# Optimization experiments

Hardware: AMD Instinct MI355X
Metric: run time of the kernel (lower is better)

## Reference

```python
import jax, jax.numpy as jnp
import numpy as np
from jax import lax

V, EMB, ENH, DNH, ZD, K = 51, 64, 256, 256, 32, 512
B, T = 1024, 128


def gru_scan(xs, h0, Wih, Whh, bih, bhh, collect):
    """PyTorch-convention GRU. xs: [T,B,D], h0: [B,H]. Returns (ys or None, hT)."""
    def step(h, x):
        gi = x @ Wih.T + bih          # [B, 3H]
        gh = h @ Whh.T + bhh          # [B, 3H]
        ir, iz, inn = jnp.split(gi, 3, axis=-1)
        hr, hz, hn = jnp.split(gh, 3, axis=-1)
        r = jax.nn.sigmoid(ir + hr)
        zg = jax.nn.sigmoid(iz + hz)
        n = jnp.tanh(inn + r * hn)
        hnew = (1.0 - zg) * n + zg * h
        return hnew, (hnew if collect else None)
    hT, ys = lax.scan(step, h0, xs)
    return ys, hT


def setup_inputs() -> dict:
    key = jax.random.key(0)
    ks = jax.random.split(key, 24)
    w = lambda k, shape, s=0.1: (jax.random.normal(k, shape, jnp.float32) * s)
    inp = {
        "x": jax.random.randint(ks[0], (B, T), 0, V),
        "emb_enc": w(ks[1], (V, EMB)),
        "emb_dec": w(ks[2], (V, EMB)),
        # encoder bidirectional GRU (fwd + bwd directions)
        "Wih_f": w(ks[3], (3 * ENH, EMB)), "Whh_f": w(ks[4], (3 * ENH, ENH)),
        "bih_f": w(ks[5], (3 * ENH,)), "bhh_f": w(ks[6], (3 * ENH,)),
        "Wih_b": w(ks[7], (3 * ENH, EMB)), "Whh_b": w(ks[8], (3 * ENH, ENH)),
        "bih_b": w(ks[9], (3 * ENH,)), "bhh_b": w(ks[10], (3 * ENH,)),
        # down_to_z: Linear(2*ENC_NH -> Z_NH)
        "Wdown": w(ks[11], (ZD, 2 * ENH)), "bdown": w(ks[12], (ZD,)),
        # VQ codebook, uniform(-1/K, 1/K) as in source
        "codebook": jax.random.uniform(ks[13], (K, ZD), jnp.float32, -1.0 / K, 1.0 / K),
        # up_from_z: Linear(Z_NH -> DEC_NH)
        "Wup": w(ks[14], (DNH, ZD)), "bup": w(ks[15], (DNH,)),
        # decoder GRU: input = INPUT_EMB_DIM + Z_NH
        "Wih_d": w(ks[16], (3 * DNH, EMB + ZD)), "Whh_d": w(ks[17], (3 * DNH, DNH)),
        "bih_d": w(ks[18], (3 * DNH,)), "bhh_d": w(ks[19], (3 * DNH,)),
        # output projection Linear(DEC_NH -> VOCABSIZE)
        "Wout": w(ks[20], (V, DNH)), "bout": w(ks[21], (V,)),
    }
    return inp


def reference(x, emb_enc, emb_dec, Wih_f, Whh_f, bih_f, bhh_f,
              Wih_b, Whh_b, bih_b, bhh_b, Wdown, bdown, codebook,
              Wup, bup, Wih_d, Whh_d, bih_d, bhh_d, Wout, bout):
    sg = lax.stop_gradient
    Bsz, Tlen = x.shape

    # ---- Encoder: bidirectional GRU, keep final hidden of each direction ----
    e = emb_enc[x]                              # [B,T,EMB]
    xs = jnp.transpose(e, (1, 0, 2))            # [T,B,EMB]
    h0 = jnp.zeros((Bsz, ENH), e.dtype)
    _, hf = gru_scan(xs, h0, Wih_f, Whh_f, bih_f, bhh_f, collect=False)
    _, hb = gru_scan(xs[::-1], h0, Wih_b, Whh_b, bih_b, bhh_b, collect=False)
    out_h = jnp.concatenate([hf, hb], axis=-1)  # [B, 2*ENH]

    # ---- down to z ----
    z = out_h @ Wdown.T + bdown                 # [B, ZD]

    # ---- VQ quantizer ----
    d2 = (z ** 2).sum(-1, keepdims=True) + (codebook ** 2).sum(-1) - 2.0 * (z @ codebook.T)  # [B,K]
    idx = jnp.argmin(d2, axis=-1)               # [B]
    quantized = codebook[idx]                   # [B, ZD]
    commit = ((sg(quantized) - z) ** 2).mean(-1)
    embed_l = ((quantized - sg(z)) ** 2).mean(-1)
    qloss = 0.1 * commit + 0.1 * embed_l
    Q = jnp.sum(qloss)
    qz = z + sg(quantized - z)                  # straight-through [B, ZD]

    # ---- up to decoder hidden ----
    hidden = qz @ Wup.T + bup                   # [B, DNH]

    # ---- Decoder GRU over src, z concatenated at every step ----
    src, tgt = x[:, :-1], x[:, 1:]
    d = emb_dec[src]                            # [B,T-1,EMB]
    zrep = jnp.broadcast_to(qz[:, None, :], (Bsz, Tlen - 1, ZD))
    dec_in = jnp.concatenate([zrep, d], axis=-1)            # [B,T-1,EMB+ZD]
    ys, _ = gru_scan(jnp.transpose(dec_in, (1, 0, 2)), hidden,
                     Wih_d, Whh_d, bih_d, bhh_d, collect=True)  # [T-1,B,DNH]
    logits = jnp.transpose(ys, (1, 0, 2)) @ Wout.T + bout   # [B,T-1,V]

    # cross entropy, reduction='sum', ignore_index=0
    logp = jax.nn.log_softmax(logits, axis=-1)
    nll = -jnp.take_along_axis(logp, tgt[..., None], axis=-1).squeeze(-1)  # [B,T-1]
    mask = (tgt != 0)
    xloss = jnp.sum(nll * mask)
    nonpadded_tokens = jnp.sum(mask)
    pred_tokens = jnp.argmax(logits, axis=-1)

    return (xloss, nonpadded_tokens, pred_tokens, Q, idx[:, None])
```

## Files before the change

### kernel.cpp

```cpp
#include <hip/hip_runtime.h>
#include <cstdint>

typedef unsigned short u16;
typedef unsigned int u32;
typedef __attribute__((ext_vector_type(4))) int int4v;
typedef __attribute__((ext_vector_type(8))) short short8;
typedef __attribute__((ext_vector_type(4))) float f32x4;

#define XLOSS_OFF 0
#define NPAD_OFF  1
#define PRED_OFF  2
#define Q_OFF     130050
#define IDX_OFF   130051

__device__ __forceinline__ u16 f2b(float f){
  union { float f; unsigned int i; } c; c.f = f;
  unsigned int i = c.i;
  unsigned int r = (i + 0x7FFFu + ((i >> 16) & 1u)) >> 16;
  return (u16)r;
}

#define LOG2E 1.442695040889634f
__device__ __forceinline__ float fast_sigmoid(float x){
  return __builtin_amdgcn_rcpf(1.f + __builtin_amdgcn_exp2f(-LOG2E*x));
}
__device__ __forceinline__ float fast_tanh(float x){
  return 1.f - 2.f*__builtin_amdgcn_rcpf(1.f + __builtin_amdgcn_exp2f((2.f*LOG2E)*x));
}

__global__ __launch_bounds__(256) void k_prep_wo(
    const float* __restrict__ Wo, u16* __restrict__ oWo, float* __restrict__ dout){
  int idx = blockIdx.x*256 + threadIdx.x;
  if (idx == 0){ dout[XLOSS_OFF]=0.f; dout[NPAD_OFF]=0.f; dout[Q_OFF]=0.f; }
  int row = idx >> 8, k = idx & 255;
  oWo[idx] = (row < 51) ? f2b(Wo[row*256 + k]) : (u16)0;
}

__global__ __launch_bounds__(64) void k_prep_q(
    const float* __restrict__ Wf, const float* __restrict__ Wb, const float* __restrict__ Wd,
    signed char* __restrict__ qf, signed char* __restrict__ qb, signed char* __restrict__ qd,
    float* __restrict__ invf, float* __restrict__ invb, float* __restrict__ invd){
  const int row = blockIdx.x;
  const int mat = row / 768, r = row - mat*768;
  const float* W = (mat==0 ? Wf : (mat==1 ? Wb : Wd)) + (size_t)r*256;
  signed char* q = (mat==0 ? qf : (mat==1 ? qb : qd)) + (size_t)r*256;
  float* inv     = (mat==0 ? invf : (mat==1 ? invb : invd));
  const int lane = threadIdx.x;
  float4 v = *(const float4*)(W + lane*4);
  float m = fmaxf(fmaxf(fabsf(v.x),fabsf(v.y)), fmaxf(fabsf(v.z),fabsf(v.w)));
  #pragma unroll
  for (int off=32; off>0; off>>=1) m = fmaxf(m, __shfl_xor(m, off));
  m = fmaxf(m, 1e-20f);
  const float s = 127.f / m;
  int a0 = __float2int_rn(v.x*s), a1 = __float2int_rn(v.y*s);
  int a2 = __float2int_rn(v.z*s), a3 = __float2int_rn(v.w*s);
  u32 packed = (a0&255) | ((a1&255)<<8) | ((a2&255)<<16) | ((a3&255)<<24);
  *(u32*)(q + lane*4) = packed;
  if (lane == 0) inv[r] = m * (1.f/127.f);
}

__global__ __launch_bounds__(256) void k_prep_g(
    const float* __restrict__ emb_e, const float* __restrict__ emb_d,
    const float* __restrict__ Wih_f, const float* __restrict__ bih_f, const float* __restrict__ bhh_f,
    const float* __restrict__ Wih_b, const float* __restrict__ bih_b, const float* __restrict__ bhh_b,
    const float* __restrict__ Wih_d,
    float* __restrict__ Gf, float* __restrict__ Gb, float* __restrict__ Gd){
  int idx = blockIdx.x*256 + threadIdx.x;
  int tab = idx / 39168;
  int rem = idx - tab*39168;
  int v = rem / 768;
  int n = rem - v*768;
  float acc = 0.f;
  if (tab == 0){
    const float* e = emb_e + v*64; const float* w = Wih_f + n*64;
    for (int k=0;k<64;k++) acc += e[k]*w[k];
    acc += bih_f[n] + (n < 512 ? bhh_f[n] : 0.f);
    Gf[rem] = acc;
  } else if (tab == 1){
    const float* e = emb_e + v*64; const float* w = Wih_b + n*64;
    for (int k=0;k<64;k++) acc += e[k]*w[k];
    acc += bih_b[n] + (n < 512 ? bhh_b[n] : 0.f);
    Gb[rem] = acc;
  } else {
    const float* e = emb_d + v*64; const float* w = Wih_d + n*96 + 32;
    for (int k=0;k<64;k++) acc += e[k]*w[k];
    Gd[rem] = acc;
  }
}

template<int MODE>
__global__ __launch_bounds__(512)
__attribute__((amdgpu_waves_per_eu(2, 2)))
void k_gru(
    const signed char* __restrict__ W0, const signed char* __restrict__ W1,
    const float* __restrict__ I0, const float* __restrict__ I1,
    const float* __restrict__ G0, const float* __restrict__ G1,
    const float* __restrict__ bhh0, const float* __restrict__ bhh1,
    const int* __restrict__ x,
    const float* __restrict__ zc, const float* __restrict__ h0g,
    float* __restrict__ out_h, u16* __restrict__ ys){
  __shared__ signed char hbf[2*4096];
  __shared__ int xsh[1024];
  __shared__ int gh[8*772];
  __shared__ float zcs[(MODE==1) ? 8*768 : 4];

  const int tid = threadIdx.x;
  const int lane = tid & 63;
  const int wave = tid >> 6;
  const int l15 = lane & 15, lhi = lane >> 4;

  bool fwd = true; int gb;
  const signed char* W; const float* G; const float* bhh; const float* invS;
  if (MODE == 0){
    int bi = blockIdx.x;
    fwd = bi < 128; gb = fwd ? bi : bi - 128;
    W = fwd ? W0 : W1; G = fwd ? G0 : G1; bhh = fwd ? bhh0 : bhh1;
    invS = fwd ? I0 : I1;
  } else {
    gb = blockIdx.x; W = W0; G = G0; bhh = bhh0; invS = I0;
  }
  const int b0 = gb * 8;
  const int nT = (MODE == 0) ? 128 : 127;
  const float HS    = (MODE == 0) ? 127.f : 63.f;
  const float invHS = (MODE == 0) ? (1.f/127.f) : (1.f/63.f);

  int4v wq[6][4];
  #pragma unroll
  for (int g=0; g<3; g++){
    #pragma unroll
    for (int hh=0; hh<2; hh++){
      const signed char* p = W + (size_t)(g*256 + wave*32 + hh*16 + l15)*256 + lhi*16;
      #pragma unroll
      for (int kt=0; kt<4; kt++)
        wq[g*2+hh][kt] = *(const int4v*)(p + kt*64);
    }
  }
  #pragma unroll
  for (int kt=0; kt<4; kt++){
    asm volatile("" : "+v"(wq[0][kt]));
    asm volatile("" : "+v"(wq[1][kt]));
    asm volatile("" : "+v"(wq[2][kt]));
    asm volatile("" : "+v"(wq[3][kt]));
    asm volatile("" : "+v"(wq[4][kt]));
    asm volatile("" : "+v"(wq[5][kt]));
  }

  const int gm = wave;
  const int c4 = lane * 4;
  f32x4 isr4 = *(const f32x4*)(invS + c4);
  f32x4 isz4 = *(const f32x4*)(invS + 256 + c4);
  f32x4 isn4 = *(const f32x4*)(invS + 512 + c4);
  #pragma unroll
  for (int i=0;i<4;i++){ isr4[i] *= invHS; isz4[i] *= invHS; isn4[i] *= invHS; }
  const f32x4 bn4 = *(const f32x4*)(bhh + 512 + c4);

  for (int i = tid; i < 1024; i += 512) xsh[i] = x[b0*128 + i];
  for (int i = tid*4; i < 8192; i += 2048) *(int*)&hbf[i] = 0;
  if (MODE == 1){
    const f32x4* src = (const f32x4*)(zc + (size_t)b0*768);
    f32x4* dst = (f32x4*)zcs;
    for (int i = tid; i < 1536; i += 512) dst[i] = src[i];
  }
  __syncthreads();

  float hreg[4];
  #pragma unroll
  for (int i=0;i<4;i++) hreg[i] = 0.f;
  if (MODE == 1){
    f32x4 h0v = *(const f32x4*)(h0g + (size_t)(b0+gm)*256 + c4);
    u32 pk = 0;
    #pragma unroll
    for (int i=0;i<4;i++){
      hreg[i] = h0v[i];
      int q = __float2int_rn(fminf(fmaxf(h0v[i]*HS, -127.f), 127.f));
      pk |= (u32)(q & 255) << (8*i);
    }
    *(u32*)&hbf[gm*256 + (c4 ^ (gm<<4))] = pk;
  }
  __syncthreads();

  int aoff[4];
  #pragma unroll
  for (int kt=0; kt<4; kt++)
    aoff[kt] = l15*256 + ((kt*64 + lhi*16) ^ (l15<<4));

  int cur = 0;
  for (int t=0; t<nT; ++t){
    const int te = (MODE==0 && !fwd) ? (127 - t) : t;
    const int tok = xsh[(gm<<7) + te];
    const float* Gp = G + (size_t)tok*768 + c4;
    f32x4 gr4 = *(const f32x4*)(Gp);
    f32x4 gz4 = *(const f32x4*)(Gp + 256);
    f32x4 gn4 = *(const f32x4*)(Gp + 512);

    const signed char* hb = hbf + (cur<<12);
    int4v af[4];
    #pragma unroll
    for (int kt=0; kt<4; kt++) af[kt] = *(const int4v*)(hb + aoff[kt]);

    int4v acc[6];
    #pragma unroll
    for (int j=0;j<6;j++) acc[j] = (int4v){0,0,0,0};
    #pragma unroll
    for (int kt=0; kt<4; kt++)
      #pragma unroll
      for (int j=0;j<6;j++)
        acc[j] = __builtin_amdgcn_mfma_i32_16x16x64_i8(af[kt], wq[j][kt], acc[j], 0,0,0);

    if (lhi < 2){
      #pragma unroll
      for (int j=0;j<6;j++){
        const int g = j >> 1;
        const int col = wave*32 + (j&1)*16 + l15;
        #pragma unroll
        for (int r=0;r<4;r++)
          gh[(4*lhi+r)*772 + g*256 + col] = acc[j][r];
      }
    }
    __syncthreads();

    int4v hiR = *(const int4v*)&gh[gm*772 + c4];
    int4v hiZ = *(const int4v*)&gh[gm*772 + 256 + c4];
    int4v hiN = *(const int4v*)&gh[gm*772 + 512 + c4];
    f32x4 zr4 = {0.f,0.f,0.f,0.f}, zz4 = zr4, zn4 = zr4;
    if (MODE == 1){
      zr4 = *(const f32x4*)&zcs[gm*768 + c4];
      zz4 = *(const f32x4*)&zcs[gm*768 + 256 + c4];
      zn4 = *(const f32x4*)&zcs[gm*768 + 512 + c4];
    }
    u32 pk = 0;
    #pragma unroll
    for (int i=0;i<4;i++){
      float gr = gr4[i] + zr4[i];
      float gz = gz4[i] + zz4[i];
      float gn = gn4[i] + zn4[i];
      float rg = fast_sigmoid((float)hiR[i]*isr4[i] + gr);
      float zg = fast_sigmoid((float)hiZ[i]*isz4[i] + gz);
      float nn = fast_tanh(gn + rg*((float)hiN[i]*isn4[i] + bn4[i]));
      float hv = nn + zg*(hreg[i] - nn);
      hreg[i] = hv;
      int q = __float2int_rn(fminf(fmaxf(hv*HS, -127.f), 127.f));
      pk |= (u32)(q & 255) << (8*i);
    }
    *(u32*)&hbf[((cur^1)<<12) + gm*256 + (c4 ^ (gm<<4))] = pk;
    if (MODE == 1){
      u32 lo = (u32)f2b(hreg[0]) | ((u32)f2b(hreg[1]) << 16);
      u32 hi = (u32)f2b(hreg[2]) | ((u32)f2b(hreg[3]) << 16);
      uint2 v; v.x = lo; v.y = hi;
      *(uint2*)&ys[((size_t)(b0+gm)*127 + t)*256 + c4] = v;
    }
    __syncthreads();
    cur ^= 1;
  }

  if (MODE == 0){
    f32x4 o = {hreg[0], hreg[1], hreg[2], hreg[3]};
    *(f32x4*)(out_h + (size_t)(b0+gm)*512 + (fwd ? 0 : 256) + c4) = o;
  }
}

__global__ __launch_bounds__(64) void k_vq(
    const float* __restrict__ outH, const float* __restrict__ Wdown, const float* __restrict__ bdown,
    const float* __restrict__ cb, const float* __restrict__ Wup, const float* __restrict__ bup,
    const float* __restrict__ Wihd, const float* __restrict__ bihd, const float* __restrict__ bhhd,
    float* __restrict__ hidden, float* __restrict__ zc, float* __restrict__ dout){
  const int b = blockIdx.x;
  const int lane = threadIdx.x;
  __shared__ float oh[512];
  __shared__ float zsh[32];
  __shared__ float qsh[32];
  {
    const float* src = outH + (size_t)b*512 + lane*8;
    *(float4*)&oh[lane*8]   = *(const float4*)src;
    *(float4*)&oh[lane*8+4] = *(const float4*)(src+4);
  }
  __syncthreads();
  if (lane < 32){
    float acc = bdown[lane];
    const float* wr = Wdown + lane*512;
    for (int k=0;k<512;k++) acc += wr[k]*oh[k];
    zsh[lane] = acc;
  }
  __syncthreads();
  float bd = 3.4e38f; int bi = 0;
  for (int c8=0;c8<8;c8++){
    const int c = lane*8 + c8;
    const float* cr = cb + c*32;
    float d = 0.f;
    #pragma unroll
    for (int k=0;k<32;k++){ float df = zsh[k]-cr[k]; d += df*df; }
    if (d < bd){ bd = d; bi = c; }
  }
  #pragma unroll
  for (int offm=32; offm>0; offm>>=1){
    float od = __shfl_xor(bd, offm);
    int   oi = __shfl_xor(bi, offm);
    if (od < bd || (od == bd && oi < bi)){ bd = od; bi = oi; }
  }
  if (lane == 0){
    atomicAdd(&dout[Q_OFF], bd * (0.2f/32.f));
    dout[IDX_OFF + b] = (float)bi;
  }
  if (lane < 32) qsh[lane] = cb[(size_t)bi*32 + lane];
  __syncthreads();
  #pragma unroll
  for (int i=0;i<4;i++){
    const int o = lane*4 + i;
    float acc = bup[o];
    const float* wr = Wup + o*32;
    #pragma unroll
    for (int k=0;k<32;k++) acc += wr[k]*qsh[k];
    hidden[(size_t)b*256 + o] = acc;
  }
  #pragma unroll
  for (int i=0;i<12;i++){
    const int o = lane*12 + i;
    float acc = bihd[o] + (o < 512 ? bhhd[o] : 0.f);
    const float* wr = Wihd + (size_t)o*96;
    #pragma unroll
    for (int k=0;k<32;k++) acc += wr[k]*qsh[k];
    zc[(size_t)b*768 + o] = acc;
  }
}

__global__ __launch_bounds__(256) void k_out(
    const u16* __restrict__ ys, const u16* __restrict__ Wo,
    const float* __restrict__ bout, const int* __restrict__ x,
    float* __restrict__ dout){
  const int tid = threadIdx.x;
  const int w = tid >> 6, lane = tid & 63;
  const int l15 = lane & 15, lhi = lane >> 4;
  __shared__ float lg[4][32][66];
  const int rows0 = blockIdx.x*128 + w*32;
  const f32x4 fz = {0.f,0.f,0.f,0.f};
  #pragma unroll
  for (int mt=0; mt<2; mt++){
    const int rb = rows0 + mt*16;
    f32x4 acc[4];
    #pragma unroll
    for (int nt=0;nt<4;nt++) acc[nt] = fz;
    #pragma unroll
    for (int kt=0; kt<8; kt++){
      short8 a = *(const short8*)&ys[(size_t)(rb + l15)*256 + kt*32 + lhi*8];
      #pragma unroll
      for (int nt=0; nt<4; nt++){
        short8 bb = *(const short8*)&Wo[(size_t)(nt*16 + l15)*256 + kt*32 + lhi*8];
        acc[nt] = __builtin_amdgcn_mfma_f32_16x16x32_bf16(a, bb, acc[nt], 0, 0, 0);
      }
    }
    #pragma unroll
    for (int nt=0;nt<4;nt++){
      const int col = nt*16 + l15;
      const float bo = (col < 51) ? bout[col] : 0.f;
      #pragma unroll
      for (int r=0;r<4;r++){
        float v = (col < 51) ? (acc[nt][r] + bo) : -1e30f;
        lg[w][mt*16 + lhi*4 + r][col] = v;
      }
    }
  }
  __syncthreads();
  float xl = 0.f, ct = 0.f;
  if (lane < 32){
    const int grow = rows0 + lane;
    const float* Lr = &lg[w][lane][0];
    float m = Lr[0]; int am = 0;
    for (int i=1;i<51;i++){ float v = Lr[i]; if (v > m){ m = v; am = i; } }
    float s = 0.f;
    for (int i=0;i<51;i++) s += __expf(Lr[i] - m);
    const int bb = grow / 127;
    const int tt = grow - bb*127;
    const int tgt = x[bb*128 + tt + 1];
    const float nll = (m + __logf(s)) - Lr[tgt];
    const float mk = (tgt != 0) ? 1.f : 0.f;
    dout[PRED_OFF + grow] = (float)am;
    xl = nll * mk; ct = mk;
  }
  #pragma unroll
  for (int off=32; off>0; off>>=1){
    xl += __shfl_xor(xl, off);
    ct += __shfl_xor(ct, off);
  }
  if (lane == 0){
    atomicAdd(&dout[XLOSS_OFF], xl);
    atomicAdd(&dout[NPAD_OFF], ct);
  }
}

extern "C" void kernel_launch(void* const* d_in, const int* in_sizes, int n_in,
                              void* d_out, int out_size, void* d_ws, size_t ws_size,
                              hipStream_t stream){
  (void)in_sizes; (void)n_in; (void)out_size; (void)ws_size;
  const int*   x      = (const int*)  d_in[0];
  const float* emb_e  = (const float*)d_in[1];
  const float* emb_d  = (const float*)d_in[2];
  const float* Wih_f  = (const float*)d_in[3];
  const float* Whh_f  = (const float*)d_in[4];
  const float* bih_f  = (const float*)d_in[5];
  const float* bhh_f  = (const float*)d_in[6];
  const float* Wih_b  = (const float*)d_in[7];
  const float* Whh_b  = (const float*)d_in[8];
  const float* bih_b  = (const float*)d_in[9];
  const float* bhh_b  = (const float*)d_in[10];
  const float* Wdown  = (const float*)d_in[11];
  const float* bdown  = (const float*)d_in[12];
  const float* cbook  = (const float*)d_in[13];
  const float* Wup    = (const float*)d_in[14];
  const float* bup    = (const float*)d_in[15];
  const float* Wih_d  = (const float*)d_in[16];
  const float* Whh_d  = (const float*)d_in[17];
  const float* bih_d  = (const float*)d_in[18];
  const float* bhh_d  = (const float*)d_in[19];
  const float* Wout   = (const float*)d_in[20];
  const float* bout   = (const float*)d_in[21];
  float* dout = (float*)d_out;

  char* ws = (char*)d_ws;
  size_t off = 0;
  auto nxt = [&](size_t bytes)->char*{
    char* r = ws + off;
    off += (bytes + 255) & ~(size_t)255;
    return r;
  };
  signed char* Wq_f = (signed char*)nxt((size_t)196608);
  signed char* Wq_b = (signed char*)nxt((size_t)196608);
  signed char* Wq_d = (signed char*)nxt((size_t)196608);
  float* invF = (float*)nxt((size_t)768*4);
  float* invB = (float*)nxt((size_t)768*4);
  float* invD = (float*)nxt((size_t)768*4);
  float* Gf    = (float*)nxt((size_t)39168*4);
  float* Gb    = (float*)nxt((size_t)39168*4);
  float* Gd    = (float*)nxt((size_t)39168*4);
  u16*   Wo_bf = (u16*) nxt((size_t)16384*2);
  float* outH  = (float*)nxt((size_t)524288*4);
  float* hid   = (float*)nxt((size_t)262144*4);
  float* zcw   = (float*)nxt((size_t)786432*4);
  u16*   ysb   = (u16*)  nxt((size_t)33292288*2);

  hipLaunchKernelGGL(k_prep_wo, dim3(64), dim3(256), 0, stream, Wout, Wo_bf, dout);
  hipLaunchKernelGGL(k_prep_q, dim3(2304), dim3(64), 0, stream,
                     Whh_f, Whh_b, Whh_d, Wq_f, Wq_b, Wq_d, invF, invB, invD);
  hipLaunchKernelGGL(k_prep_g, dim3(459), dim3(256), 0, stream,
                     emb_e, emb_d, Wih_f, bih_f, bhh_f, Wih_b, bih_b, bhh_b, Wih_d,
                     Gf, Gb, Gd);
  hipLaunchKernelGGL((k_gru<0>), dim3(256), dim3(512), 0, stream,
                     Wq_f, Wq_b, invF, invB, Gf, Gb, bhh_f, bhh_b, x,
                     (const float*)nullptr, (const float*)nullptr, outH, (u16*)nullptr);
  hipLaunchKernelGGL(k_vq, dim3(1024), dim3(64), 0, stream,
                     outH, Wdown, bdown, cbook, Wup, bup, Wih_d, bih_d, bhh_d,
                     hid, zcw, dout);
  hipLaunchKernelGGL((k_gru<1>), dim3(128), dim3(512), 0, stream,
                     Wq_d, (const signed char*)nullptr, invD, (const float*)nullptr,
                     Gd, (const float*)nullptr, bhh_d, (const float*)nullptr, x,
                     zcw, hid, (float*)nullptr, ysb);
  hipLaunchKernelGGL(k_out, dim3(1016), dim3(256), 0, stream,
                     ysb, Wo_bf, bout, x, dout);
}
```

Baseline: 531.6 us.

## Ping-pong two batch groups per GRU block to overlap MFMA with gate math

The GRU kernel now splits each block's batch rows into two groups, A and B, each with its own hidden-state and gate buffers in shared memory. The recurrent MFMA for one group is issued while the other group runs its sigmoid/tanh gate update, so matrix and vector work can overlap across the per-step barrier. The decoder now uses 2 rows per group and twice as many blocks, to spread its work over more CUs. The cost is that each MFMA tile only fills 2–4 of its 16 rows, and gate outputs and bf16 ys are written per element instead of as packed vector stores.

```diff
diff --git a/kernel.cpp b/kernel.cpp
--- a/kernel.cpp
+++ b/kernel.cpp
@@ -88,7 +88,7 @@
   }
 }
 
-template<int MODE>
+template<int MODE, int GR>
 __global__ __launch_bounds__(512)
 __attribute__((amdgpu_waves_per_eu(2, 2)))
 void k_gru(
@@ -99,10 +99,14 @@
     const int* __restrict__ x,
     const float* __restrict__ zc, const float* __restrict__ h0g,
     float* __restrict__ out_h, u16* __restrict__ ys){
-  __shared__ signed char hbf[2*4096];
-  __shared__ int xsh[1024];
-  __shared__ int gh[8*772];
-  __shared__ float zcs[(MODE==1) ? 8*768 : 4];
+  constexpr int TPR = 512 / GR;
+  constexpr int CPL = 256 / TPR;
+
+  __shared__ signed char hbfA[2*4096];
+  __shared__ signed char hbfB[2*4096];
+  __shared__ int xsh[2*GR*128];
+  __shared__ int ghA[GR*772], ghB[GR*772];
+  __shared__ float zcs[(MODE==1) ? 2*GR*768 : 4];
 
   const int tid = threadIdx.x;
   const int lane = tid & 63;
@@ -112,14 +116,15 @@
   bool fwd = true; int gb;
   const signed char* W; const float* G; const float* bhh; const float* invS;
   if (MODE == 0){
+    const int nblk = 1024 / (2*GR);
     int bi = blockIdx.x;
-    fwd = bi < 128; gb = fwd ? bi : bi - 128;
+    fwd = bi < nblk; gb = fwd ? bi : bi - nblk;
     W = fwd ? W0 : W1; G = fwd ? G0 : G1; bhh = fwd ? bhh0 : bhh1;
     invS = fwd ? I0 : I1;
   } else {
     gb = blockIdx.x; W = W0; G = G0; bhh = bhh0; invS = I0;
   }
-  const int b0 = gb * 8;
+  const int b0 = gb * (2*GR);
   const int nT = (MODE == 0) ? 128 : 127;
   const float HS    = (MODE == 0) ? 127.f : 63.f;
   const float invHS = (MODE == 0) ? (1.f/127.f) : (1.f/63.f);
@@ -145,37 +150,41 @@
     asm volatile("" : "+v"(wq[5][kt]));
   }
 
-  const int gm = wave;
-  const int c4 = lane * 4;
-  f32x4 isr4 = *(const f32x4*)(invS + c4);
-  f32x4 isz4 = *(const f32x4*)(invS + 256 + c4);
-  f32x4 isn4 = *(const f32x4*)(invS + 512 + c4);
-  #pragma unroll
-  for (int i=0;i<4;i++){ isr4[i] *= invHS; isz4[i] *= invHS; isn4[i] *= invHS; }
-  const f32x4 bn4 = *(const f32x4*)(bhh + 512 + c4);
-
-  for (int i = tid; i < 1024; i += 512) xsh[i] = x[b0*128 + i];
-  for (int i = tid*4; i < 8192; i += 2048) *(int*)&hbf[i] = 0;
+  const int gm = tid / TPR;
+  const int ci = (tid % TPR) * CPL;
+  float isr[CPL], isz[CPL], isn[CPL], bnv[CPL];
+  #pragma unroll
+  for (int i=0;i<CPL;i++){
+    isr[i] = invS[ci+i]       * invHS;
+    isz[i] = invS[256 + ci+i] * invHS;
+    isn[i] = invS[512 + ci+i] * invHS;
+    bnv[i] = bhh[512 + ci+i];
+  }
+
+  for (int i = tid; i < 2*GR*128; i += 512) xsh[i] = x[b0*128 + i];
+  for (int i = tid*4; i < 8192; i += 2048){
+    *(int*)&hbfA[i] = 0; *(int*)&hbfB[i] = 0;
+  }
   if (MODE == 1){
     const f32x4* src = (const f32x4*)(zc + (size_t)b0*768);
     f32x4* dst = (f32x4*)zcs;
-    for (int i = tid; i < 1536; i += 512) dst[i] = src[i];
-  }
-  __syncthreads();
-
-  float hreg[4];
-  #pragma unroll
-  for (int i=0;i<4;i++) hreg[i] = 0.f;
+    for (int i = tid; i < 2*GR*192; i += 512) dst[i] = src[i];
+  }
+  __syncthreads();
+
+  float hA[CPL], hB[CPL];
+  #pragma unroll
+  for (int i=0;i<CPL;i++){ hA[i]=0.f; hB[i]=0.f; }
   if (MODE == 1){
-    f32x4 h0v = *(const f32x4*)(h0g + (size_t)(b0+gm)*256 + c4);
-    u32 pk = 0;
-    #pragma unroll
-    for (int i=0;i<4;i++){
-      hreg[i] = h0v[i];
-      int q = __float2int_rn(fminf(fmaxf(h0v[i]*HS, -127.f), 127.f));
-      pk |= (u32)(q & 255) << (8*i);
-    }
-    *(u32*)&hbf[gm*256 + (c4 ^ (gm<<4))] = pk;
+    #pragma unroll
+    for (int i=0;i<CPL;i++){
+      hA[i] = h0g[(size_t)(b0+gm)*256 + ci+i];
+      hB[i] = h0g[(size_t)(b0+GR+gm)*256 + ci+i];
+      int qa = __float2int_rn(fminf(fmaxf(hA[i]*HS, -127.f), 127.f));
+      int qb = __float2int_rn(fminf(fmaxf(hB[i]*HS, -127.f), 127.f));
+      hbfA[gm*256 + ((ci+i) ^ (gm<<4))] = (signed char)qa;
+      hbfB[gm*256 + ((ci+i) ^ (gm<<4))] = (signed char)qb;
+    }
   }
   __syncthreads();
 
@@ -184,79 +193,100 @@
   for (int kt=0; kt<4; kt++)
     aoff[kt] = l15*256 + ((kt*64 + lhi*16) ^ (l15<<4));
 
-  int cur = 0;
+  #define DO_MFMA(HB, GH) do { \
+    const signed char* hb_ = (HB); \
+    int4v af_[4]; \
+    _Pragma("unroll") for (int kt=0; kt<4; kt++) af_[kt] = *(const int4v*)(hb_ + aoff[kt]); \
+    int4v acc_[6]; \
+    _Pragma("unroll") for (int j=0;j<6;j++) acc_[j] = (int4v){0,0,0,0}; \
+    _Pragma("unroll") for (int kt=0; kt<4; kt++){ \
+      _Pragma("unroll") for (int j=0;j<6;j++) \
+        acc_[j] = __builtin_amdgcn_mfma_i32_16x16x64_i8(af_[kt], wq[j][kt], acc_[j], 0,0,0); \
+    } \
+    if (lhi == 0){ \
+      _Pragma("unroll") for (int j=0;j<6;j++){ \
+        const int g_ = j >> 1; \
+        const int col_ = wave*32 + (j&1)*16 + l15; \
+        _Pragma("unroll") for (int r=0;r<GR;r++) \
+          (GH)[r*772 + g_*256 + col_] = acc_[j][r]; \
+      } \
+    } \
+  } while(0)
+
+  #define DO_GATE(GH, H, XROW, HBDST, SWROW) do { \
+    int hiR_[CPL], hiZ_[CPL], hiN_[CPL]; \
+    _Pragma("unroll") for (int i=0;i<CPL;i++){ \
+      hiR_[i] = (GH)[gm*772 + ci+i]; \
+      hiZ_[i] = (GH)[gm*772 + 256 + ci+i]; \
+      hiN_[i] = (GH)[gm*772 + 512 + ci+i]; \
+    } \
+    _Pragma("unroll") for (int i=0;i<CPL;i++){ \
+      float rg = fast_sigmoid((float)hiR_[i]*isr[i] + gvr[i]); \
+      float zg = fast_sigmoid((float)hiZ_[i]*isz[i] + gvz[i]); \
+      float nn = fast_tanh(gvn[i] + rg*((float)hiN_[i]*isn[i] + bnv[i])); \
+      float hv = nn + zg*((H)[i] - nn); \
+      (H)[i] = hv; \
+      int q_ = __float2int_rn(fminf(fmaxf(hv*HS, -127.f), 127.f)); \
+      (HBDST)[gm*256 + ((ci+i) ^ ((SWROW)<<4))] = (signed char)q_; \
+      if (MODE == 1) ys[((size_t)(b0+(XROW))*127 + t)*256 + ci+i] = f2b(hv); \
+    } \
+  } while(0)
+
+  int curA = 0, curB = 0;
+
+  DO_MFMA(hbfA + (curA<<12), ghA);
+  __syncthreads();
+
   for (int t=0; t<nT; ++t){
     const int te = (MODE==0 && !fwd) ? (127 - t) : t;
-    const int tok = xsh[(gm<<7) + te];
-    const float* Gp = G + (size_t)tok*768 + c4;
-    f32x4 gr4 = *(const f32x4*)(Gp);
-    f32x4 gz4 = *(const f32x4*)(Gp + 256);
-    f32x4 gn4 = *(const f32x4*)(Gp + 512);
-
-    const signed char* hb = hbf + (cur<<12);
-    int4v af[4];
-    #pragma unroll
-    for (int kt=0; kt<4; kt++) af[kt] = *(const int4v*)(hb + aoff[kt]);
-
-    int4v acc[6];
-    #pragma unroll
-    for (int j=0;j<6;j++) acc[j] = (int4v){0,0,0,0};
-    #pragma unroll
-    for (int kt=0; kt<4; kt++)
+
+    {
+      const int tokA = xsh[gm*128 + te];
+      const float* GpA = G + (size_t)tokA*768 + ci;
+      float gvr[CPL], gvz[CPL], gvn[CPL];
       #pragma unroll
-      for (int j=0;j<6;j++)
-        acc[j] = __builtin_amdgcn_mfma_i32_16x16x64_i8(af[kt], wq[j][kt], acc[j], 0,0,0);
-
-    if (lhi < 2){
+      for (int i=0;i<CPL;i++){
+        gvr[i] = GpA[i]; gvz[i] = GpA[256+i]; gvn[i] = GpA[512+i];
+        if (MODE == 1){
+          gvr[i] += zcs[gm*768 + ci+i];
+          gvz[i] += zcs[gm*768 + 256 + ci+i];
+          gvn[i] += zcs[gm*768 + 512 + ci+i];
+        }
+      }
+      DO_MFMA(hbfB + (curB<<12), ghB);
+      DO_GATE(ghA, hA, gm, (hbfA + ((curA^1)<<12)), gm);
+    }
+    __syncthreads();
+
+    {
+      const int tokB = xsh[(GR+gm)*128 + te];
+      const float* GpB = G + (size_t)tokB*768 + ci;
+      float gvr[CPL], gvz[CPL], gvn[CPL];
       #pragma unroll
-      for (int j=0;j<6;j++){
-        const int g = j >> 1;
-        const int col = wave*32 + (j&1)*16 + l15;
-        #pragma unroll
-        for (int r=0;r<4;r++)
-          gh[(4*lhi+r)*772 + g*256 + col] = acc[j][r];
+      for (int i=0;i<CPL;i++){
+        gvr[i] = GpB[i]; gvz[i] = GpB[256+i]; gvn[i] = GpB[512+i];
+        if (MODE == 1){
+          gvr[i] += zcs[(GR+gm)*768 + ci+i];
+          gvz[i] += zcs[(GR+gm)*768 + 256 + ci+i];
+          gvn[i] += zcs[(GR+gm)*768 + 512 + ci+i];
+        }
       }
+      if (t < nT-1) DO_MFMA(hbfA + ((curA^1)<<12), ghA);
+      DO_GATE(ghB, hB, (GR+gm), (hbfB + ((curB^1)<<12)), gm);
     }
     __syncthreads();
-
-    int4v hiR = *(const int4v*)&gh[gm*772 + c4];
-    int4v hiZ = *(const int4v*)&gh[gm*772 + 256 + c4];
-    int4v hiN = *(const int4v*)&gh[gm*772 + 512 + c4];
-    f32x4 zr4 = {0.f,0.f,0.f,0.f}, zz4 = zr4, zn4 = zr4;
-    if (MODE == 1){
-      zr4 = *(const f32x4*)&zcs[gm*768 + c4];
-      zz4 = *(const f32x4*)&zcs[gm*768 + 256 + c4];
-      zn4 = *(const f32x4*)&zcs[gm*768 + 512 + c4];
-    }
-    u32 pk = 0;
-    #pragma unroll
-    for (int i=0;i<4;i++){
-      float gr = gr4[i] + zr4[i];
-      float gz = gz4[i] + zz4[i];
-      float gn = gn4[i] + zn4[i];
-      float rg = fast_sigmoid((float)hiR[i]*isr4[i] + gr);
-      float zg = fast_sigmoid((float)hiZ[i]*isz4[i] + gz);
-      float nn = fast_tanh(gn + rg*((float)hiN[i]*isn4[i] + bn4[i]));
-      float hv = nn + zg*(hreg[i] - nn);
-      hreg[i] = hv;
-      int q = __float2int_rn(fminf(fmaxf(hv*HS, -127.f), 127.f));
-      pk |= (u32)(q & 255) << (8*i);
-    }
-    *(u32*)&hbf[((cur^1)<<12) + gm*256 + (c4 ^ (gm<<4))] = pk;
-    if (MODE == 1){
-      u32 lo = (u32)f2b(hreg[0]) | ((u32)f2b(hreg[1]) << 16);
-      u32 hi = (u32)f2b(hreg[2]) | ((u32)f2b(hreg[3]) << 16);
-      uint2 v; v.x = lo; v.y = hi;
-      *(uint2*)&ys[((size_t)(b0+gm)*127 + t)*256 + c4] = v;
-    }
-    __syncthreads();
-    cur ^= 1;
+    curA ^= 1; curB ^= 1;
   }
 
   if (MODE == 0){
-    f32x4 o = {hreg[0], hreg[1], hreg[2], hreg[3]};
-    *(f32x4*)(out_h + (size_t)(b0+gm)*512 + (fwd ? 0 : 256) + c4) = o;
-  }
+    #pragma unroll
+    for (int i=0;i<CPL;i++){
+      out_h[(size_t)(b0+gm)*512    + (fwd ? 0 : 256) + ci+i] = hA[i];
+      out_h[(size_t)(b0+GR+gm)*512 + (fwd ? 0 : 256) + ci+i] = hB[i];
+    }
+  }
+  #undef DO_MFMA
+  #undef DO_GATE
 }
 
 __global__ __launch_bounds__(64) void k_vq(
@@ -443,13 +473,13 @@
   hipLaunchKernelGGL(k_prep_g, dim3(459), dim3(256), 0, stream,
                      emb_e, emb_d, Wih_f, bih_f, bhh_f, Wih_b, bih_b, bhh_b, Wih_d,
                      Gf, Gb, Gd);
-  hipLaunchKernelGGL((k_gru<0>), dim3(256), dim3(512), 0, stream,
+  hipLaunchKernelGGL((k_gru<0,4>), dim3(256), dim3(512), 0, stream,
                      Wq_f, Wq_b, invF, invB, Gf, Gb, bhh_f, bhh_b, x,
                      (const float*)nullptr, (const float*)nullptr, outH, (u16*)nullptr);
   hipLaunchKernelGGL(k_vq, dim3(1024), dim3(64), 0, stream,
                      outH, Wdown, bdown, cbook, Wup, bup, Wih_d, bih_d, bhh_d,
                      hid, zcw, dout);
-  hipLaunchKernelGGL((k_gru<1>), dim3(128), dim3(512), 0, stream,
+  hipLaunchKernelGGL((k_gru<1,2>), dim3(256), dim3(512), 0, stream,
                      Wq_d, (const signed char*)nullptr, invD, (const float*)nullptr,
                      Gd, (const float*)nullptr, bhh_d, (const float*)nullptr, x,
                      zcw, hid, (float*)nullptr, ysb);
```

Measured after the change: 605.5 us. +13.9%, slower.

## Split decoder GRU across more blocks by processing four batch rows per block

Applied to the files above, without the earlier changes.

The GRU kernel is templated on the number of batch rows per block. The decoder GRU now runs 4 rows per block across 256 blocks instead of 8 rows across 128, so more CUs share the serial recurrence. Each thread handles two hidden columns instead of four. The int8 MFMA tiles still cover 16 rows, so half of the matrix work is wasted. Element-wise stores of bytes and scalars replace the vectorized packed stores, which could add LDS and global traffic.

```diff
diff --git a/kernel.cpp b/kernel.cpp
--- a/kernel.cpp
+++ b/kernel.cpp
@@ -88,7 +88,7 @@
   }
 }
 
-template<int MODE>
+template<int MODE, int ROWS>
 __global__ __launch_bounds__(512)
 __attribute__((amdgpu_waves_per_eu(2, 2)))
 void k_gru(
@@ -99,10 +99,13 @@
     const int* __restrict__ x,
     const float* __restrict__ zc, const float* __restrict__ h0g,
     float* __restrict__ out_h, u16* __restrict__ ys){
+  constexpr int TPR = 512 / ROWS;
+  constexpr int CPL = 256 / TPR;
+
   __shared__ signed char hbf[2*4096];
-  __shared__ int xsh[1024];
-  __shared__ int gh[8*772];
-  __shared__ float zcs[(MODE==1) ? 8*768 : 4];
+  __shared__ int xsh[ROWS*128];
+  __shared__ int gh[ROWS*772];
+  __shared__ float zcs[(MODE==1) ? ROWS*768 : 4];
 
   const int tid = threadIdx.x;
   const int lane = tid & 63;
@@ -112,14 +115,15 @@
   bool fwd = true; int gb;
   const signed char* W; const float* G; const float* bhh; const float* invS;
   if (MODE == 0){
+    const int nblk = 1024 / ROWS;
     int bi = blockIdx.x;
-    fwd = bi < 128; gb = fwd ? bi : bi - 128;
+    fwd = bi < nblk; gb = fwd ? bi : bi - nblk;
     W = fwd ? W0 : W1; G = fwd ? G0 : G1; bhh = fwd ? bhh0 : bhh1;
     invS = fwd ? I0 : I1;
   } else {
     gb = blockIdx.x; W = W0; G = G0; bhh = bhh0; invS = I0;
   }
-  const int b0 = gb * 8;
+  const int b0 = gb * ROWS;
   const int nT = (MODE == 0) ? 128 : 127;
   const float HS    = (MODE == 0) ? 127.f : 63.f;
   const float invHS = (MODE == 0) ? (1.f/127.f) : (1.f/63.f);
@@ -145,37 +149,37 @@
     asm volatile("" : "+v"(wq[5][kt]));
   }
 
-  const int gm = wave;
-  const int c4 = lane * 4;
-  f32x4 isr4 = *(const f32x4*)(invS + c4);
-  f32x4 isz4 = *(const f32x4*)(invS + 256 + c4);
-  f32x4 isn4 = *(const f32x4*)(invS + 512 + c4);
-  #pragma unroll
-  for (int i=0;i<4;i++){ isr4[i] *= invHS; isz4[i] *= invHS; isn4[i] *= invHS; }
-  const f32x4 bn4 = *(const f32x4*)(bhh + 512 + c4);
-
-  for (int i = tid; i < 1024; i += 512) xsh[i] = x[b0*128 + i];
+  const int gm = tid / TPR;
+  const int ci = (tid % TPR) * CPL;
+  float isr[CPL], isz[CPL], isn[CPL], bnv[CPL];
+  #pragma unroll
+  for (int i=0;i<CPL;i++){
+    isr[i] = invS[ci+i]       * invHS;
+    isz[i] = invS[256 + ci+i] * invHS;
+    isn[i] = invS[512 + ci+i] * invHS;
+    bnv[i] = bhh[512 + ci+i];
+  }
+
+  for (int i = tid; i < ROWS*128; i += 512) xsh[i] = x[b0*128 + i];
   for (int i = tid*4; i < 8192; i += 2048) *(int*)&hbf[i] = 0;
   if (MODE == 1){
     const f32x4* src = (const f32x4*)(zc + (size_t)b0*768);
     f32x4* dst = (f32x4*)zcs;
-    for (int i = tid; i < 1536; i += 512) dst[i] = src[i];
-  }
-  __syncthreads();
-
-  float hreg[4];
-  #pragma unroll
-  for (int i=0;i<4;i++) hreg[i] = 0.f;
+    for (int i = tid; i < ROWS*192; i += 512) dst[i] = src[i];
+  }
+  __syncthreads();
+
+  float hreg[CPL];
+  #pragma unroll
+  for (int i=0;i<CPL;i++) hreg[i] = 0.f;
   if (MODE == 1){
-    f32x4 h0v = *(const f32x4*)(h0g + (size_t)(b0+gm)*256 + c4);
-    u32 pk = 0;
-    #pragma unroll
-    for (int i=0;i<4;i++){
-      hreg[i] = h0v[i];
-      int q = __float2int_rn(fminf(fmaxf(h0v[i]*HS, -127.f), 127.f));
-      pk |= (u32)(q & 255) << (8*i);
-    }
-    *(u32*)&hbf[gm*256 + (c4 ^ (gm<<4))] = pk;
+    #pragma unroll
+    for (int i=0;i<CPL;i++){
+      float hv = h0g[(size_t)(b0+gm)*256 + ci+i];
+      hreg[i] = hv;
+      int q = __float2int_rn(fminf(fmaxf(hv*HS, -127.f), 127.f));
+      hbf[gm*256 + ((ci+i) ^ (gm<<4))] = (signed char)q;
+    }
   }
   __syncthreads();
 
@@ -188,10 +192,12 @@
   for (int t=0; t<nT; ++t){
     const int te = (MODE==0 && !fwd) ? (127 - t) : t;
     const int tok = xsh[(gm<<7) + te];
-    const float* Gp = G + (size_t)tok*768 + c4;
-    f32x4 gr4 = *(const f32x4*)(Gp);
-    f32x4 gz4 = *(const f32x4*)(Gp + 256);
-    f32x4 gn4 = *(const f32x4*)(Gp + 512);
+    const float* Gp = G + (size_t)tok*768 + ci;
+    float gvr[CPL], gvz[CPL], gvn[CPL];
+    #pragma unroll
+    for (int i=0;i<CPL;i++){
+      gvr[i] = Gp[i]; gvz[i] = Gp[256+i]; gvn[i] = Gp[512+i];
+    }
 
     const signed char* hb = hbf + (cur<<12);
     int4v af[4];
@@ -207,7 +213,7 @@
       for (int j=0;j<6;j++)
         acc[j] = __builtin_amdgcn_mfma_i32_16x16x64_i8(af[kt], wq[j][kt], acc[j], 0,0,0);
 
-    if (lhi < 2){
+    if (4*lhi < ROWS){
       #pragma unroll
       for (int j=0;j<6;j++){
         const int g = j >> 1;
@@ -219,43 +225,50 @@
     }
     __syncthreads();
 
-    int4v hiR = *(const int4v*)&gh[gm*772 + c4];
-    int4v hiZ = *(const int4v*)&gh[gm*772 + 256 + c4];
-    int4v hiN = *(const int4v*)&gh[gm*772 + 512 + c4];
-    f32x4 zr4 = {0.f,0.f,0.f,0.f}, zz4 = zr4, zn4 = zr4;
+    int hiR[CPL], hiZ[CPL], hiN[CPL];
+    #pragma unroll
+    for (int i=0;i<CPL;i++){
+      hiR[i] = gh[gm*772 + ci+i];
+      hiZ[i] = gh[gm*772 + 256 + ci+i];
+      hiN[i] = gh[gm*772 + 512 + ci+i];
+    }
     if (MODE == 1){
-      zr4 = *(const f32x4*)&zcs[gm*768 + c4];
-      zz4 = *(const f32x4*)&zcs[gm*768 + 256 + c4];
-      zn4 = *(const f32x4*)&zcs[gm*768 + 512 + c4];
-    }
-    u32 pk = 0;
-    #pragma unroll
-    for (int i=0;i<4;i++){
-      float gr = gr4[i] + zr4[i];
-      float gz = gz4[i] + zz4[i];
-      float gn = gn4[i] + zn4[i];
-      float rg = fast_sigmoid((float)hiR[i]*isr4[i] + gr);
-      float zg = fast_sigmoid((float)hiZ[i]*isz4[i] + gz);
-      float nn = fast_tanh(gn + rg*((float)hiN[i]*isn4[i] + bn4[i]));
+      #pragma unroll
+      for (int i=0;i<CPL;i++){
+        gvr[i] += zcs[gm*768 + ci+i];
+        gvz[i] += zcs[gm*768 + 256 + ci+i];
+        gvn[i] += zcs[gm*768 + 512 + ci+i];
+      }
+    }
+    #pragma unroll
+    for (int i=0;i<CPL;i++){
+      float rg = fast_sigmoid((float)hiR[i]*isr[i] + gvr[i]);
+      float zg = fast_sigmoid((float)hiZ[i]*isz[i] + gvz[i]);
+      float nn = fast_tanh(gvn[i] + rg*((float)hiN[i]*isn[i] + bnv[i]));
       float hv = nn + zg*(hreg[i] - nn);
       hreg[i] = hv;
       int q = __float2int_rn(fminf(fmaxf(hv*HS, -127.f), 127.f));
-      pk |= (u32)(q & 255) << (8*i);
-    }
-    *(u32*)&hbf[((cur^1)<<12) + gm*256 + (c4 ^ (gm<<4))] = pk;
+      hbf[((cur^1)<<12) + gm*256 + ((ci+i) ^ (gm<<4))] = (signed char)q;
+    }
     if (MODE == 1){
-      u32 lo = (u32)f2b(hreg[0]) | ((u32)f2b(hreg[1]) << 16);
-      u32 hi = (u32)f2b(hreg[2]) | ((u32)f2b(hreg[3]) << 16);
-      uint2 v; v.x = lo; v.y = hi;
-      *(uint2*)&ys[((size_t)(b0+gm)*127 + t)*256 + c4] = v;
+      if constexpr (CPL == 2){
+        u32 v = (u32)f2b(hreg[0]) | ((u32)f2b(hreg[1]) << 16);
+        *(u32*)&ys[((size_t)(b0+gm)*127 + t)*256 + ci] = v;
+      } else {
+        u32 lo = (u32)f2b(hreg[0]) | ((u32)f2b(hreg[1]) << 16);
+        u32 hi = (u32)f2b(hreg[2]) | ((u32)f2b(hreg[3]) << 16);
+        uint2 v; v.x = lo; v.y = hi;
+        *(uint2*)&ys[((size_t)(b0+gm)*127 + t)*256 + ci] = v;
+      }
     }
     __syncthreads();
     cur ^= 1;
   }
 
   if (MODE == 0){
-    f32x4 o = {hreg[0], hreg[1], hreg[2], hreg[3]};
-    *(f32x4*)(out_h + (size_t)(b0+gm)*512 + (fwd ? 0 : 256) + c4) = o;
+    #pragma unroll
+    for (int i=0;i<CPL;i++)
+      out_h[(size_t)(b0+gm)*512 + (fwd ? 0 : 256) + ci+i] = hreg[i];
   }
 }
 
@@ -443,13 +456,13 @@
   hipLaunchKernelGGL(k_prep_g, dim3(459), dim3(256), 0, stream,
                      emb_e, emb_d, Wih_f, bih_f, bhh_f, Wih_b, bih_b, bhh_b, Wih_d,
                      Gf, Gb, Gd);
-  hipLaunchKernelGGL((k_gru<0>), dim3(256), dim3(512), 0, stream,
+  hipLaunchKernelGGL((k_gru<0,8>), dim3(256), dim3(512), 0, stream,
                      Wq_f, Wq_b, invF, invB, Gf, Gb, bhh_f, bhh_b, x,
                      (const float*)nullptr, (const float*)nullptr, outH, (u16*)nullptr);
   hipLaunchKernelGGL(k_vq, dim3(1024), dim3(64), 0, stream,
                      outH, Wdown, bdown, cbook, Wup, bup, Wih_d, bih_d, bhh_d,
                      hid, zcw, dout);
-  hipLaunchKernelGGL((k_gru<1>), dim3(128), dim3(512), 0, stream,
+  hipLaunchKernelGGL((k_gru<1,4>), dim3(256), dim3(512), 0, stream,
                      Wq_d, (const signed char*)nullptr, invD, (const float*)nullptr,
                      Gd, (const float*)nullptr, bhh_d, (const float*)nullptr, x,
                      zcw, hid, (float*)nullptr, ysb);
```

Result: faster. 491.4 us (-7.6%).
